# Kernel tuning notes

Measured on AMD Instinct MI355X. Metric: run time of the kernel, lower is better.

The kernel has to match this reference:

```python
import jax, jax.numpy as jnp
import numpy as np

EMBED_DIM = 128
NUM_SYMBOLS = 200000
PAD_IDX = NUM_SYMBOLS
K_NEIGHBORS = 10
PROCESS_STEPS = 4
D_MODEL = 2 * EMBED_DIM   # 256
D_INNER = 2 * D_MODEL     # 512
LSTM_HID = 2 * D_MODEL    # 512
B, F_SUP, MAX_K = 4096, 5, 64


def setup_inputs() -> dict:
    key = jax.random.key(0)
    ks = jax.random.split(key, 40)
    f = lambda i, shape, s=0.05: jax.random.normal(ks[i], shape, jnp.float32) * s
    inp = {}
    inp['query'] = jax.random.randint(ks[0], (B, 2), 0, NUM_SYMBOLS)
    inp['support'] = jax.random.randint(ks[1], (F_SUP, 2), 0, NUM_SYMBOLS)
    inp['q_l1'] = jax.random.randint(ks[2], (B, MAX_K, 2), 0, NUM_SYMBOLS + 1)
    inp['q_deg_l'] = jax.random.randint(ks[3], (B,), 0, 100)
    inp['q_r1'] = jax.random.randint(ks[4], (B, MAX_K, 2), 0, NUM_SYMBOLS + 1)
    inp['q_deg_r'] = jax.random.randint(ks[5], (B,), 0, 100)
    inp['s_l1'] = jax.random.randint(ks[6], (F_SUP, MAX_K, 2), 0, NUM_SYMBOLS + 1)
    inp['s_deg_l'] = jax.random.randint(ks[7], (F_SUP,), 0, 100)
    inp['s_r1'] = jax.random.randint(ks[8], (F_SUP, MAX_K, 2), 0, NUM_SYMBOLS + 1)
    inp['s_deg_r'] = jax.random.randint(ks[9], (F_SUP,), 0, 100)
    # learned parameters
    inp['symbol_emb'] = f(10, (NUM_SYMBOLS + 1, EMBED_DIM), 0.1).at[PAD_IDX].set(0.0)
    inp['gcn_w_w'] = f(11, (EMBED_DIM, 2 * EMBED_DIM))
    inp['gcn_w_b'] = jnp.zeros((EMBED_DIM,), jnp.float32)
    inp['gcn_b'] = jnp.zeros((EMBED_DIM,), jnp.float32)
    inp['g1_w'] = f(12, (EMBED_DIM // 2, EMBED_DIM))
    inp['g1_b'] = jnp.zeros((EMBED_DIM // 2,), jnp.float32)
    inp['ln1_g'] = jnp.ones((EMBED_DIM // 2,), jnp.float32)
    inp['ln1_b'] = jnp.zeros((EMBED_DIM // 2,), jnp.float32)
    inp['g2_w'] = f(13, (1, EMBED_DIM // 2))
    inp['g2_b'] = jnp.zeros((1,), jnp.float32)
    inp['gate_temp'] = jnp.array(1.0, jnp.float32)
    inp['se_p1_w'] = f(14, (D_INNER, D_MODEL))
    inp['se_p1_b'] = jnp.zeros((D_INNER,), jnp.float32)
    inp['se_p2_w'] = f(15, (D_MODEL, D_INNER))
    inp['se_p2_b'] = jnp.zeros((D_MODEL,), jnp.float32)
    inp['se_ln_g'] = jnp.ones((D_MODEL,), jnp.float32)
    inp['se_ln_b'] = jnp.zeros((D_MODEL,), jnp.float32)
    inp['w_ih'] = f(16, (4 * LSTM_HID, D_MODEL))
    inp['w_hh'] = f(17, (4 * LSTM_HID, LSTM_HID))
    inp['b_ih'] = jnp.zeros((4 * LSTM_HID,), jnp.float32)
    inp['b_hh'] = jnp.zeros((4 * LSTM_HID,), jnp.float32)
    return inp


def _layernorm(x, g, b, eps=1e-5):
    m = jnp.mean(x, axis=-1, keepdims=True)
    v = jnp.var(x, axis=-1, keepdims=True)
    return (x - m) / jnp.sqrt(v + eps) * g + b


def _l2norm(x):
    return x / jnp.maximum(jnp.linalg.norm(x, axis=-1, keepdims=True), 1e-12)


def _neighbor_encoder(conn, deg, self_ids, p):
    emb = p['symbol_emb']
    rel, ent = conn[:, :, 0], conn[:, :, 1]
    rel_emb = emb[rel]            # [n, K, D] gather
    ent_emb = emb[ent]            # [n, K, D]
    self_emb = emb[self_ids]      # [n, D]
    sim = jnp.einsum('nd,nkd->nk', _l2norm(self_emb), _l2norm(ent_emb))
    is_pad = (rel == PAD_IDX).astype(jnp.float32)
    sim = sim - is_pad * 1e9
    k = min(K_NEIGHBORS, conn.shape[1])
    _, k_idx = jax.lax.top_k(sim, k)
    bidx = jnp.arange(conn.shape[0])[:, None]
    k_mask = jnp.zeros(sim.shape, jnp.float32).at[bidx, k_idx].set(1.0)[..., None]
    concat = jnp.concatenate([rel_emb, ent_emb], axis=-1)   # [n, K, 2D]
    proj = jax.nn.leaky_relu(concat @ p['gcn_w_w'].T + p['gcn_w_b'] + p['gcn_b'], 0.01)
    valid = (1.0 - is_pad[..., None]) * k_mask
    denom = jnp.maximum(jnp.sum(valid, axis=1), 1.0)
    agg = jnp.sum((proj * k_mask) * valid, axis=1) / denom   # [n, D]
    h = jax.nn.relu(_layernorm(agg @ p['g1_w'].T + p['g1_b'], p['ln1_g'], p['ln1_b']))
    logit = h @ p['g2_w'].T + p['g2_b']                      # [n, 1]
    temp = jnp.clip(p['gate_temp'], 0.1, 5.0)
    gate = jax.nn.sigmoid(logit / temp) * (deg > 0).astype(jnp.float32)[:, None]
    return jnp.tanh(self_emb + gate * agg)


def _support_encoder(x, p):
    h = jax.nn.relu(x @ p['se_p1_w'].T + p['se_p1_b'])
    h = h @ p['se_p2_w'].T + p['se_p2_b']
    return _layernorm(h + x, p['se_ln_g'], p['se_ln_b'])


def _query_encoder(support, query, p):
    n = query.shape[0]
    h_r0 = jnp.zeros((n, LSTM_HID), jnp.float32)
    c0 = jnp.zeros((n, LSTM_HID), jnp.float32)

    def step(carry, _):
        h_r, c = carry
        gates = query @ p['w_ih'].T + p['b_ih'] + h_r @ p['w_hh'].T + p['b_hh']
        i, f, g, o = jnp.split(gates, 4, axis=-1)
        c = jax.nn.sigmoid(f) * c + jax.nn.sigmoid(i) * jnp.tanh(g)
        h_ = jax.nn.sigmoid(o) * jnp.tanh(c)
        h = query + h_[:, :D_MODEL]
        attn = jax.nn.softmax(h @ support.T, axis=1)
        r = attn @ support
        return (jnp.concatenate([h, r], axis=-1), c), None

    (h_r, _), _ = jax.lax.scan(step, (h_r0, c0), None, length=PROCESS_STEPS)
    return h_r[:, :D_MODEL]


def reference(query, support, q_l1, q_deg_l, q_r1, q_deg_r, s_l1, s_deg_l, s_r1, s_deg_r,
              symbol_emb, gcn_w_w, gcn_w_b, gcn_b, g1_w, g1_b, ln1_g, ln1_b, g2_w, g2_b,
              gate_temp, se_p1_w, se_p1_b, se_p2_w, se_p2_b, se_ln_g, se_ln_b,
              w_ih, w_hh, b_ih, b_hh):
    p = dict(symbol_emb=symbol_emb, gcn_w_w=gcn_w_w, gcn_w_b=gcn_w_b, gcn_b=gcn_b,
             g1_w=g1_w, g1_b=g1_b, ln1_g=ln1_g, ln1_b=ln1_b, g2_w=g2_w, g2_b=g2_b,
             gate_temp=gate_temp, se_p1_w=se_p1_w, se_p1_b=se_p1_b, se_p2_w=se_p2_w,
             se_p2_b=se_p2_b, se_ln_g=se_ln_g, se_ln_b=se_ln_b,
             w_ih=w_ih, w_hh=w_hh, b_ih=b_ih, b_hh=b_hh)
    q_left = _neighbor_encoder(q_l1, q_deg_l, query[:, 0], p)
    q_right = _neighbor_encoder(q_r1, q_deg_r, query[:, 1], p)
    query_vec = jnp.concatenate([q_left, q_right], axis=-1)      # [B, 2D]
    s_left = _neighbor_encoder(s_l1, s_deg_l, support[:, 0], p)
    s_right = _neighbor_encoder(s_r1, s_deg_r, support[:, 1], p)
    support_vec = jnp.concatenate([s_left, s_right], axis=-1)    # [F, 2D]
    support_g = jnp.mean(_support_encoder(support_vec, p), axis=0, keepdims=True)  # [1, 2D]
    query_enc = _support_encoder(query_vec, p)                   # [B, 2D]
    query_g = _query_encoder(support_g, query_enc, p)            # [B, 2D]
    return jnp.sum(query_g * support_g, axis=1)                  # [B]
```

## Files before the change

kernel.cpp:

```cpp
#include <hip/hip_runtime.h>
#include <math.h>

#define BQ 4096
#define F_SUP 5
#define MAXK 64
#define ED 128
#define DM 256
#define DI 512
#define LH 512
#define NG 2048
#define PADX 200000
#define KNB 10
#define MROWS 82048
#define MREAL 82020
#define MQ 4224

typedef unsigned short u16;
typedef __attribute__((ext_vector_type(8))) short short8;
typedef __attribute__((ext_vector_type(4))) float floatx4;

__device__ __forceinline__ float sigf(float x) { return 1.0f / (1.0f + __expf(-x)); }
__device__ __forceinline__ float tanh_fast(float x) {
  float a = fabsf(x);
  float e = __expf(-2.0f * a);
  float t = (1.0f - e) / (1.0f + e);
  return copysignf(t, x);
}
__device__ __forceinline__ u16 f2bf(float f) {
  unsigned u = __float_as_uint(f);
  unsigned r = (u + 0x7FFFu + ((u >> 16) & 1u)) >> 16;
  return (u16)r;
}
__device__ __forceinline__ float bf2f(u16 u) {
  return __uint_as_float(((unsigned)u) << 16);
}
__device__ __forceinline__ void gl2lds16(const void* g, void* l) {
  __builtin_amdgcn_global_load_lds(
      (const __attribute__((address_space(1))) void*)g,
      (__attribute__((address_space(3))) void*)l, 16, 0, 0);
}

__global__ __launch_bounds__(256) void nbr_topk_kernel(
    const int* __restrict__ query, const int* __restrict__ support,
    const int* __restrict__ q_l1, const int* __restrict__ q_r1,
    const int* __restrict__ s_l1, const int* __restrict__ s_r1,
    const float* __restrict__ emb,
    int* __restrict__ idxA, int* __restrict__ meta)
{
  __shared__ int relS[64], entS[64];
  __shared__ __align__(16) float sE[128];
  __shared__ float simS[64];
  __shared__ int selS[16];
  __shared__ int cntS;
  __shared__ float nsS;

  int tid = threadIdx.x;
  int b = blockIdx.x;
  const int* conn; int self_id;
  if (b < BQ)              { int i = b;              conn = q_l1 + i*(MAXK*2); self_id = query[2*i];   }
  else if (b < 2*BQ)       { int i = b - BQ;         conn = q_r1 + i*(MAXK*2); self_id = query[2*i+1]; }
  else if (b < 2*BQ+F_SUP) { int i = b - 2*BQ;       conn = s_l1 + i*(MAXK*2); self_id = support[2*i]; }
  else                     { int i = b - 2*BQ-F_SUP; conn = s_r1 + i*(MAXK*2); self_id = support[2*i+1]; }

  if (tid < 128) {
    int v = conn[tid];
    if (tid & 1) entS[tid >> 1] = v; else relS[tid >> 1] = v;
    sE[tid] = emb[(long)self_id * ED + tid];
  }
  __syncthreads();
  if (tid < 64) {
    float v = sE[tid]*sE[tid] + sE[tid+64]*sE[tid+64];
    #pragma unroll
    for (int off = 1; off < 64; off <<= 1) v += __shfl_xor(v, off);
    if (tid == 0) nsS = fmaxf(sqrtf(v), 1e-12f);
  }
  __syncthreads();

  {
    int k = tid >> 2, part = tid & 3;
    const float* er = emb + (long)entS[k] * ED + part * 32;
    const float* sr = &sE[part * 32];
    float dot = 0.f, sq = 0.f;
    #pragma unroll
    for (int j = 0; j < 32; j += 4) {
      float4 e = *(const float4*)(er + j);
      float4 s = *(const float4*)(sr + j);
      dot += e.x*s.x + e.y*s.y + e.z*s.z + e.w*s.w;
      sq  += e.x*e.x + e.y*e.y + e.z*e.z + e.w*e.w;
    }
    dot += __shfl_xor(dot, 1); dot += __shfl_xor(dot, 2);
    sq  += __shfl_xor(sq, 1);  sq  += __shfl_xor(sq, 2);
    if (part == 0) {
      float ne = fmaxf(sqrtf(sq), 1e-12f);
      float sim = dot / (nsS * ne);
      if (relS[k] == PADX) sim -= 1e9f;
      simS[k] = sim;
    }
  }
  __syncthreads();

  if (tid < 64) {
    float mys = simS[tid];
    int rank = 0;
    #pragma unroll
    for (int j = 0; j < 64; ++j) {
      float s = simS[j];
      rank += ((s > mys) || (s == mys && j < tid)) ? 1 : 0;
    }
    bool val = (rank < KNB) && (relS[tid] != PADX);
    unsigned long long vm = __ballot(val ? 1 : 0);
    if (val) {
      int pos = __popcll(vm & ((1ull << tid) - 1ull));
      selS[pos] = tid;
    }
    if (tid == 0) { cntS = __popcll(vm); meta[b] = __popcll(vm); }
  }
  __syncthreads();

  int cnt = cntS;
  long base = (long)b * 10;
  if (tid < 2 * KNB) {
    int kk = tid >> 1, h = tid & 1;
    int id = PADX;
    if (kk < cnt) { int k = selS[kk]; id = h ? entS[k] : relS[k]; }
    idxA[(base + kk) * 2 + h] = id;
  }
  if (b == 0 && tid >= 128 && tid < 128 + 2 * (MROWS - MREAL)) {
    idxA[(long)MREAL * 2 + (tid - 128)] = PADX;
  }
}

__global__ __launch_bounds__(256) void proj_gather_gemm(
    const int* __restrict__ idxA, const float* __restrict__ emb,
    const u16* __restrict__ W, u16* __restrict__ proj)
{
  __shared__ u16 As[128 * 32];
  __shared__ u16 Bs[128 * 32];
  __shared__ int idxS[256];
  int tid = threadIdx.x;
  int bm = blockIdx.x;
  idxS[tid] = idxA[bm * 256 + tid];
  int lane = tid & 63, wave = tid >> 6;
  int wm = (wave & 1) * 64, wn = (wave >> 1) * 64;
  int col = lane & 15, quad = lane >> 4;
  int r = tid >> 1, part = tid & 1;

  floatx4 acc[4][4];
  #pragma unroll
  for (int i = 0; i < 4; ++i)
    #pragma unroll
    for (int j = 0; j < 4; ++j) { floatx4 z = {0.f,0.f,0.f,0.f}; acc[i][j] = z; }
  __syncthreads();

  for (int k0 = 0; k0 < 256; k0 += 32) {
    int half = k0 >> 7, koff = k0 & 127;
    #pragma unroll
    for (int t = 0; t < 2; ++t) {
      int c = t * 256 + tid;
      int rb = c >> 2, o = c & 3;
      int og = o ^ (rb & 3);
      gl2lds16(W + (long)rb * 256 + k0 + og * 8, &Bs[(size_t)c * 8]);
    }
    {
      int id = idxS[r * 2 + half];
      const float* src = emb + (long)id * ED + koff + part * 16;
      float4 f0 = *(const float4*)(src);
      float4 f1 = *(const float4*)(src + 4);
      float4 f2 = *(const float4*)(src + 8);
      float4 f3 = *(const float4*)(src + 12);
      short8 s0, s1;
      s0[0]=(short)f2bf(f0.x); s0[1]=(short)f2bf(f0.y); s0[2]=(short)f2bf(f0.z); s0[3]=(short)f2bf(f0.w);
      s0[4]=(short)f2bf(f1.x); s0[5]=(short)f2bf(f1.y); s0[6]=(short)f2bf(f1.z); s0[7]=(short)f2bf(f1.w);
      s1[0]=(short)f2bf(f2.x); s1[1]=(short)f2bf(f2.y); s1[2]=(short)f2bf(f2.z); s1[3]=(short)f2bf(f2.w);
      s1[4]=(short)f2bf(f3.x); s1[5]=(short)f2bf(f3.y); s1[6]=(short)f2bf(f3.z); s1[7]=(short)f2bf(f3.w);
      int o0 = 2 * part, o1 = 2 * part + 1;
      *(short8*)&As[(size_t)(r * 4 + (o0 ^ (r & 3))) * 8] = s0;
      *(short8*)&As[(size_t)(r * 4 + (o1 ^ (r & 3))) * 8] = s1;
    }
    __syncthreads();
    short8 af[4], bfr[4];
    #pragma unroll
    for (int i = 0; i < 4; ++i) {
      int ra = wm + i * 16 + col;
      af[i] = *(const short8*)&As[(size_t)(ra * 4 + (quad ^ (ra & 3))) * 8];
      int rb = wn + i * 16 + col;
      bfr[i] = *(const short8*)&Bs[(size_t)(rb * 4 + (quad ^ (rb & 3))) * 8];
    }
    #pragma unroll
    for (int i = 0; i < 4; ++i)
      #pragma unroll
      for (int j = 0; j < 4; ++j)
        acc[i][j] = __builtin_amdgcn_mfma_f32_16x16x32_bf16(af[i], bfr[j], acc[i][j], 0, 0, 0);
    __syncthreads();
  }
  int gm0 = bm * 128 + wm + quad * 4;
  int gn0 = wn + col;
  #pragma unroll
  for (int i = 0; i < 4; ++i)
    #pragma unroll
    for (int j = 0; j < 4; ++j)
      #pragma unroll
      for (int rr = 0; rr < 4; ++rr)
        proj[(long)(gm0 + i * 16 + rr) * 128 + gn0 + j * 16] = f2bf(acc[i][j][rr]);
}

__global__ __launch_bounds__(128) void nbr_post_kernel(
    const int* __restrict__ query, const int* __restrict__ support,
    const int* __restrict__ q_deg_l, const int* __restrict__ q_deg_r,
    const int* __restrict__ s_deg_l, const int* __restrict__ s_deg_r,
    const float* __restrict__ emb,
    const u16* __restrict__ proj, const int* __restrict__ meta,
    const float* __restrict__ gcn_w_b, const float* __restrict__ gcn_b,
    const float* __restrict__ g1_w, const float* __restrict__ g1_b,
    const float* __restrict__ ln1_g, const float* __restrict__ ln1_b,
    const float* __restrict__ g2_w, const float* __restrict__ g2_b,
    const float* __restrict__ gate_temp,
    float* __restrict__ qv, u16* __restrict__ qv_bf)
{
  __shared__ __align__(16) float aggS[128];
  __shared__ float sEs[128];
  __shared__ float gateS;
  int tid = threadIdx.x, b = blockIdx.x;
  int deg, self_id, row, colb;
  if (b < BQ)              { int i = b;              deg = q_deg_l[i]; self_id = query[2*i];     row = i;        colb = 0;  }
  else if (b < 2*BQ)       { int i = b - BQ;         deg = q_deg_r[i]; self_id = query[2*i+1];   row = i;        colb = ED; }
  else if (b < 2*BQ+F_SUP) { int i = b - 2*BQ;       deg = s_deg_l[i]; self_id = support[2*i];   row = BQ + i;   colb = 0;  }
  else                     { int i = b - 2*BQ-F_SUP; deg = s_deg_r[i]; self_id = support[2*i+1]; row = BQ + i;   colb = ED; }
  float* outp = qv + (long)row * DM + colb;
  u16*  outpb = qv_bf + (long)row * DM + colb;

  int cnt = meta[b];
  float denom = fmaxf((float)cnt, 1.0f);
  float bsum = gcn_w_b[tid] + gcn_b[tid];
  float agg = 0.f;
  long pbase = (long)b * 10;
  for (int kk = 0; kk < cnt; ++kk) {
    float z = bf2f(proj[(pbase + kk) * 128 + tid]) + bsum;
    z = (z >= 0.f) ? z : 0.01f * z;
    agg += z;
  }
  agg /= denom;
  aggS[tid] = agg;
  sEs[tid] = emb[(long)self_id * ED + tid];
  __syncthreads();

  if (tid < 64) {
    int e = tid;
    const float4* g1r = (const float4*)(g1_w + e * ED);
    float y = g1_b[e];
    #pragma unroll 8
    for (int j = 0; j < 32; ++j) {
      float4 w = g1r[j];
      float4 a = *(const float4*)&aggS[j * 4];
      y += w.x*a.x + w.y*a.y + w.z*a.z + w.w*a.w;
    }
    float s = y;
    #pragma unroll
    for (int off = 1; off < 64; off <<= 1) s += __shfl_xor(s, off);
    float mean = s * (1.0f / 64.0f);
    float dv = y - mean;
    float s2 = dv * dv;
    #pragma unroll
    for (int off = 1; off < 64; off <<= 1) s2 += __shfl_xor(s2, off);
    float var = s2 * (1.0f / 64.0f);
    float hv = dv / sqrtf(var + 1e-5f) * ln1_g[e] + ln1_b[e];
    hv = fmaxf(hv, 0.f);
    float lp = hv * g2_w[e];
    #pragma unroll
    for (int off = 1; off < 64; off <<= 1) lp += __shfl_xor(lp, off);
    if (e == 0) {
      float logit = lp + g2_b[0];
      float temp = fminf(fmaxf(gate_temp[0], 0.1f), 5.0f);
      float gate = 1.0f / (1.0f + expf(-logit / temp));
      if (deg <= 0) gate = 0.f;
      gateS = gate;
    }
  }
  __syncthreads();
  float o = tanhf(sEs[tid] + gateS * aggS[tid]);
  outp[tid] = o;
  outpb[tid] = f2bf(o);
}

__global__ __launch_bounds__(256) void mfma_gemm(
    const u16* __restrict__ A, int lda,
    const u16* __restrict__ W, int ldw,
    int N, int K,
    float* __restrict__ Cout, u16* __restrict__ Cbf,
    const float* __restrict__ bias0,
    const u16* __restrict__ gqin,
    u16* __restrict__ gqout,
    int relu, int lstm_mode,
    float* __restrict__ cstate, const float* __restrict__ qe,
    u16* __restrict__ hbf)
{
  __shared__ u16 As[128 * 32];
  __shared__ u16 Bs[128 * 32];
  int tid = threadIdx.x;
  int nb = N >> 7;
  int bn = blockIdx.x % nb, bm = blockIdx.x / nb;
  int lane = tid & 63, wave = tid >> 6;
  int wm = (wave & 1) * 64, wn = (wave >> 1) * 64;
  int col = lane & 15, quad = lane >> 4;

  u16 gqa[64]; float cpv[16]; float qev[16]; float scv[4];
  int u = 0; long fb = 0;
  if (lstm_mode) {
    u = bn * 32 + (wave >> 1) * 16 + col;
    fb = ((long)blockIdx.x * 4 + wave) * 64 + lane;
    #pragma unroll
    for (int j = 0; j < 4; ++j)
      scv[j] = bias0[bn * 128 + (wave >> 1) * 64 + j * 16 + col];
    if (lstm_mode == 1) {
      const short8* gp = (const short8*)(gqin + fb * 64);
      #pragma unroll
      for (int t = 0; t < 8; ++t) *(short8*)&gqa[t * 8] = gp[t];
      const float4* cp = (const float4*)(cstate + fb * 16);
      #pragma unroll
      for (int t = 0; t < 4; ++t) *(float4*)&cpv[t * 4] = cp[t];
    }
    if (u < DM) {
      #pragma unroll
      for (int i = 0; i < 4; ++i)
        #pragma unroll
        for (int r = 0; r < 4; ++r) {
          int m = bm * 128 + (wave & 1) * 64 + i * 16 + quad * 4 + r;
          qev[i * 4 + r] = qe[(long)m * DM + u];
        }
    }
  }

  floatx4 acc[4][4];
  #pragma unroll
  for (int i = 0; i < 4; ++i)
    #pragma unroll
    for (int j = 0; j < 4; ++j) { floatx4 z = {0.f,0.f,0.f,0.f}; acc[i][j] = z; }

  for (int k0 = 0; k0 < K; k0 += 32) {
    #pragma unroll
    for (int t = 0; t < 2; ++t) {
      int c = t * 256 + tid;
      int r = c >> 2, o = c & 3;
      int og = o ^ (r & 3);
      gl2lds16(A + (long)(bm * 128 + r) * lda + k0 + og * 8, &As[(size_t)c * 8]);
      gl2lds16(W + (long)(bn * 128 + r) * ldw + k0 + og * 8, &Bs[(size_t)c * 8]);
    }
    __syncthreads();
    short8 af[4], bfr[4];
    #pragma unroll
    for (int i = 0; i < 4; ++i) {
      int ra = wm + i * 16 + col;
      af[i] = *(const short8*)&As[(size_t)(ra * 4 + (quad ^ (ra & 3))) * 8];
      int rb = wn + i * 16 + col;
      bfr[i] = *(const short8*)&Bs[(size_t)(rb * 4 + (quad ^ (rb & 3))) * 8];
    }
    #pragma unroll
    for (int i = 0; i < 4; ++i)
      #pragma unroll
      for (int j = 0; j < 4; ++j)
        acc[i][j] = __builtin_amdgcn_mfma_f32_16x16x32_bf16(af[i], bfr[j], acc[i][j], 0, 0, 0);
    __syncthreads();
  }

  if (lstm_mode) {
    float cnew[16];
    #pragma unroll
    for (int i = 0; i < 4; ++i) {
      #pragma unroll
      for (int r = 0; r < 4; ++r) {
        float gI = acc[i][0][r] + scv[0];
        float gF = acc[i][1][r] + scv[1];
        float gG = acc[i][2][r] + scv[2];
        float gO = acc[i][3][r] + scv[3];
        if (lstm_mode == 1) {
          gI += bf2f(gqa[(i * 4 + 0) * 4 + r]);
          gF += bf2f(gqa[(i * 4 + 1) * 4 + r]);
          gG += bf2f(gqa[(i * 4 + 2) * 4 + r]);
          gO += bf2f(gqa[(i * 4 + 3) * 4 + r]);
        }
        float cp = (lstm_mode == 2) ? 0.f : cpv[i * 4 + r];
        float cn = sigf(gF) * cp + sigf(gI) * tanh_fast(gG);
        cnew[i * 4 + r] = cn;
        if (u < DM) {
          int m = bm * 128 + (wave & 1) * 64 + i * 16 + quad * 4 + r;
          hbf[(long)m * DM + u] = f2bf(qev[i * 4 + r] + sigf(gO) * tanh_fast(cn));
        }
      }
    }
    {
      float4* cp = (float4*)(cstate + fb * 16);
      #pragma unroll
      for (int t = 0; t < 4; ++t) cp[t] = *(float4*)&cnew[t * 4];
    }
    if (lstm_mode == 2) {
      u16 ga[64];
      #pragma unroll
      for (int i = 0; i < 4; ++i)
        #pragma unroll
        for (int j = 0; j < 4; ++j)
          #pragma unroll
          for (int r = 0; r < 4; ++r)
            ga[(i * 4 + j) * 4 + r] = f2bf(acc[i][j][r] + scv[j]);
      short8* gp = (short8*)(gqout + fb * 64);
      #pragma unroll
      for (int t = 0; t < 8; ++t) gp[t] = *(short8*)&ga[t * 8];
    }
  } else {
    int gm0 = bm * 128 + wm + quad * 4;
    int gn0 = bn * 128 + wn + col;
    #pragma unroll
    for (int i = 0; i < 4; ++i) {
      #pragma unroll
      for (int j = 0; j < 4; ++j) {
        int n = gn0 + j * 16;
        #pragma unroll
        for (int r = 0; r < 4; ++r) {
          int m = gm0 + i * 16 + r;
          float v = acc[i][j][r];
          if (bias0) v += bias0[n];
          if (relu) v = fmaxf(v, 0.f);
          if (Cout) Cout[(long)m * N + n] = v;
          if (Cbf)  Cbf[(long)m * N + n] = f2bf(v);
        }
      }
    }
  }
}

__global__ void prep_cast(
    const float* __restrict__ p1, const float* __restrict__ p2,
    const float* __restrict__ gcnw, const float* __restrict__ wih,
    const float* __restrict__ whh, const float* __restrict__ bih,
    const float* __restrict__ bhh,
    u16* __restrict__ p1b, u16* __restrict__ p2b, u16* __restrict__ gcnb,
    u16* __restrict__ wihb, u16* __restrict__ whhb, float* __restrict__ bihh)
{
  int gid = blockIdx.x * 256 + threadIdx.x;
  if (gid < 131072) { p1b[gid] = f2bf(p1[gid]); }
  else if (gid < 262144) { int i = gid - 131072; p2b[i] = f2bf(p2[i]); }
  else if (gid < 294912) { int i = gid - 262144; gcnb[i] = f2bf(gcnw[i]); }
  else if (gid < 819200) {
    int i = gid - 294912; int p = i >> 8, k = i & 255;
    int g = (p >> 4) & 3, uu = (p >> 7) * 32 + ((p >> 6) & 1) * 16 + (p & 15);
    int n = g * 512 + uu;
    wihb[i] = f2bf(wih[(long)n * DM + k]);
  } else if (gid < 1343488) {
    int i = gid - 819200; int p = i >> 8, k = i & 255;
    int g = (p >> 4) & 3, uu = (p >> 7) * 32 + ((p >> 6) & 1) * 16 + (p & 15);
    int n = g * 512 + uu;
    whhb[i] = f2bf(whh[(long)n * LH + k]);
  } else if (gid < 1345536) {
    int p = gid - 1343488;
    int g = (p >> 4) & 3, uu = (p >> 7) * 32 + ((p >> 6) & 1) * 16 + (p & 15);
    int n = g * 512 + uu;
    bihh[p] = bih[n] + bhh[n];
  }
}

__global__ __launch_bounds__(256) void ln_residual_kernel(
    const float* __restrict__ h2buf, const float* __restrict__ xbuf,
    const float* __restrict__ lng, const float* __restrict__ lnb,
    float* __restrict__ out, u16* __restrict__ outb)
{
  __shared__ float red[4];
  int r = blockIdx.x, tid = threadIdx.x;
  float v = h2buf[(long)r * DM + tid] + xbuf[(long)r * DM + tid];
  float s = v;
  #pragma unroll
  for (int off = 1; off < 64; off <<= 1) s += __shfl_xor(s, off);
  if ((tid & 63) == 0) red[tid >> 6] = s;
  __syncthreads();
  float mean = (red[0] + red[1] + red[2] + red[3]) * (1.0f / 256.0f);
  __syncthreads();
  float dv = v - mean;
  float s2 = dv * dv;
  #pragma unroll
  for (int off = 1; off < 64; off <<= 1) s2 += __shfl_xor(s2, off);
  if ((tid & 63) == 0) red[tid >> 6] = s2;
  __syncthreads();
  float var = (red[0] + red[1] + red[2] + red[3]) * (1.0f / 256.0f);
  float o = dv / sqrtf(var + 1e-5f) * lng[tid] + lnb[tid];
  out[(long)r * DM + tid] = o;
  outb[(long)r * DM + tid] = f2bf(o);
}

__global__ __launch_bounds__(256) void scorr_kernel(
    const float* __restrict__ qe, const float* __restrict__ whh,
    float* __restrict__ sg, float* __restrict__ s_corr_perm)
{
  __shared__ float sgS[DM];
  int tid = threadIdx.x;
  {
    float v = 0.f;
    #pragma unroll
    for (int r = 0; r < F_SUP; ++r) v += qe[(long)(BQ + r) * DM + tid];
    v *= (1.0f / (float)F_SUP);
    sgS[tid] = v;
    if (blockIdx.x == 0) sg[tid] = v;
  }
  __syncthreads();
  int wave = tid >> 6, lane = tid & 63;
  int n = blockIdx.x * 4 + wave;
  float4 w = *(const float4*)(whh + (long)n * LH + DM + lane * 4);
  float4 s = *(const float4*)&sgS[lane * 4];
  float d = w.x*s.x + w.y*s.y + w.z*s.z + w.w*s.w;
  #pragma unroll
  for (int off = 1; off < 64; off <<= 1) d += __shfl_xor(d, off);
  if (lane == 0) {
    int g = n >> 9, uu = n & 511;
    int p = (uu >> 5) * 128 + ((uu >> 4) & 1) * 64 + g * 16 + (uu & 15);
    s_corr_perm[p] = d;
  }
}

__global__ __launch_bounds__(256) void final_dot_kernel(
    const u16* __restrict__ h, const float* __restrict__ sg, float* __restrict__ out)
{
  __shared__ float red[4];
  int m = blockIdx.x, tid = threadIdx.x;
  float v = bf2f(h[(long)m * DM + tid]) * sg[tid];
  #pragma unroll
  for (int off = 1; off < 64; off <<= 1) v += __shfl_xor(v, off);
  if ((tid & 63) == 0) red[tid >> 6] = v;
  __syncthreads();
  if (tid == 0) out[m] = red[0] + red[1] + red[2] + red[3];
}

extern "C" void kernel_launch(void* const* d_in, const int* in_sizes, int n_in,
                              void* d_out, int out_size, void* d_ws, size_t ws_size,
                              hipStream_t stream)
{
  const int*   query    = (const int*)  d_in[0];
  const int*   support  = (const int*)  d_in[1];
  const int*   q_l1     = (const int*)  d_in[2];
  const int*   q_deg_l  = (const int*)  d_in[3];
  const int*   q_r1     = (const int*)  d_in[4];
  const int*   q_deg_r  = (const int*)  d_in[5];
  const int*   s_l1     = (const int*)  d_in[6];
  const int*   s_deg_l  = (const int*)  d_in[7];
  const int*   s_r1     = (const int*)  d_in[8];
  const int*   s_deg_r  = (const int*)  d_in[9];
  const float* symbol_emb = (const float*)d_in[10];
  const float* gcn_w_w  = (const float*)d_in[11];
  const float* gcn_w_b  = (const float*)d_in[12];
  const float* gcn_b    = (const float*)d_in[13];
  const float* g1_w     = (const float*)d_in[14];
  const float* g1_b     = (const float*)d_in[15];
  const float* ln1_g    = (const float*)d_in[16];
  const float* ln1_b    = (const float*)d_in[17];
  const float* g2_w     = (const float*)d_in[18];
  const float* g2_b     = (const float*)d_in[19];
  const float* gate_temp= (const float*)d_in[20];
  const float* se_p1_w  = (const float*)d_in[21];
  const float* se_p1_b  = (const float*)d_in[22];
  const float* se_p2_w  = (const float*)d_in[23];
  const float* se_p2_b  = (const float*)d_in[24];
  const float* se_ln_g  = (const float*)d_in[25];
  const float* se_ln_b  = (const float*)d_in[26];
  const float* w_ih     = (const float*)d_in[27];
  const float* w_hh     = (const float*)d_in[28];
  const float* b_ih     = (const float*)d_in[29];
  const float* b_hh     = (const float*)d_in[30];

  float* ws = (float*)d_ws;
  size_t off = 0;
  float* projF   = ws + off; off += (size_t)MROWS * 128 / 2;
  float* idxF    = ws + off; off += (size_t)MROWS * 2;
  float* qv      = ws + off; off += (size_t)MQ * DM;
  float* qe      = ws + off; off += (size_t)MQ * DM;
  float* qv_bfF  = ws + off; off += (size_t)MQ * DM / 2;
  float* qe_bfF  = ws + off; off += (size_t)MQ * DM / 2;
  float* h1bF    = ws + off; off += (size_t)MQ * DI / 2;
  float* H2      = ws + off; off += (size_t)MQ * DM;
  float* gqbF    = ws + off; off += (size_t)BQ * NG / 2;
  float* cstate  = ws + off; off += (size_t)BQ * LH;
  float* hbf0F   = ws + off; off += (size_t)BQ * DM / 2;
  float* hbf1F   = ws + off; off += (size_t)BQ * DM / 2;
  float* p1bF    = ws + off; off += 131072 / 2;
  float* p2bF    = ws + off; off += 131072 / 2;
  float* gcnbF   = ws + off; off += 32768 / 2;
  float* wihbF   = ws + off; off += 524288 / 2;
  float* whhbF   = ws + off; off += 524288 / 2;
  float* bihh    = ws + off; off += 2048;
  float* sg      = ws + off; off += 256;
  float* s_corr  = ws + off; off += 2048;
  float* metaF   = ws + off; off += 8448;

  u16* proj   = (u16*)projF;
  int* idxA   = (int*)idxF;
  u16* qv_bf  = (u16*)qv_bfF;
  u16* qe_bf  = (u16*)qe_bfF;
  u16* H1_bf  = (u16*)h1bF;
  u16* gq_fr  = (u16*)gqbF;
  u16* hbf0   = (u16*)hbf0F;
  u16* hbf1   = (u16*)hbf1F;
  u16* p1b    = (u16*)p1bF;
  u16* p2b    = (u16*)p2bF;
  u16* gcnb   = (u16*)gcnbF;
  u16* wihb   = (u16*)wihbF;
  u16* whhb   = (u16*)whhbF;
  int* meta   = (int*)metaF;

  prep_cast<<<5256, 256, 0, stream>>>(se_p1_w, se_p2_w, gcn_w_w, w_ih, w_hh, b_ih, b_hh,
                                      p1b, p2b, gcnb, wihb, whhb, bihh);

  nbr_topk_kernel<<<2 * BQ + 2 * F_SUP, 256, 0, stream>>>(
      query, support, q_l1, q_r1, s_l1, s_r1, symbol_emb, idxA, meta);

  proj_gather_gemm<<<MROWS / 128, 256, 0, stream>>>(idxA, symbol_emb, gcnb, proj);

  nbr_post_kernel<<<2 * BQ + 2 * F_SUP, 128, 0, stream>>>(
      query, support, q_deg_l, q_deg_r, s_deg_l, s_deg_r, symbol_emb,
      proj, meta, gcn_w_b, gcn_b, g1_w, g1_b, ln1_g, ln1_b, g2_w, g2_b, gate_temp,
      qv, qv_bf);

  mfma_gemm<<<(MQ / 128) * (DI / 128), 256, 0, stream>>>(qv_bf, 256, p1b, 256, DI, 256,
      nullptr, H1_bf, se_p1_b, nullptr, nullptr, 1, 0, nullptr, nullptr, nullptr);
  mfma_gemm<<<(MQ / 128) * (DM / 128), 256, 0, stream>>>(H1_bf, 512, p2b, 512, DM, 512,
      H2, nullptr, se_p2_b, nullptr, nullptr, 0, 0, nullptr, nullptr, nullptr);
  ln_residual_kernel<<<BQ + F_SUP, 256, 0, stream>>>(H2, qv, se_ln_g, se_ln_b, qe, qe_bf);

  scorr_kernel<<<512, 256, 0, stream>>>(qe, w_hh, sg, s_corr);

  mfma_gemm<<<(BQ / 128) * (NG / 128), 256, 0, stream>>>(qe_bf, 256, wihb, 256, NG, 256,
      nullptr, nullptr, bihh, nullptr, gq_fr, 0, 2, cstate, qe, hbf0);

  mfma_gemm<<<(BQ / 128) * (NG / 128), 256, 0, stream>>>(hbf0, 256, whhb, 256, NG, 256,
      nullptr, nullptr, s_corr, gq_fr, nullptr, 0, 1, cstate, qe, hbf1);
  mfma_gemm<<<(BQ / 128) * (NG / 128), 256, 0, stream>>>(hbf1, 256, whhb, 256, NG, 256,
      nullptr, nullptr, s_corr, gq_fr, nullptr, 0, 1, cstate, qe, hbf0);
  mfma_gemm<<<(BQ / 128) * (NG / 128), 256, 0, stream>>>(hbf0, 256, whhb, 256, NG, 256,
      nullptr, nullptr, s_corr, gq_fr, nullptr, 0, 1, cstate, qe, hbf1);

  final_dot_kernel<<<BQ, 256, 0, stream>>>(hbf1, sg, (float*)d_out);
}
```

Before: 427.6 us.

## Split neighbor top-k into a barrier-free similarity kernel and a wave-level rank kernel

The fused top-k kernel is split in two. The first kernel computes cosine similarities with a single barrier, interleaved coalesced float4 loads, and no division by the self-embedding norm, since a positive scale does not change the ranking. It writes the similarities to a global buffer. The second kernel ranks them with one wave per row using shuffles and writes the selected index pairs. This removes several block barriers and most idle threads, at the cost of an extra launch and a global round trip for the similarity buffer.

```diff
diff --git a/kernel.cpp b/kernel.cpp
--- a/kernel.cpp
+++ b/kernel.cpp
@@ -40,93 +40,84 @@
       (__attribute__((address_space(3))) void*)l, 16, 0, 0);
 }
 
-__global__ __launch_bounds__(256) void nbr_topk_kernel(
+__global__ __launch_bounds__(256) void nbr_sim_kernel(
     const int* __restrict__ query, const int* __restrict__ support,
     const int* __restrict__ q_l1, const int* __restrict__ q_r1,
     const int* __restrict__ s_l1, const int* __restrict__ s_r1,
-    const float* __restrict__ emb,
-    int* __restrict__ idxA, int* __restrict__ meta)
-{
-  __shared__ int relS[64], entS[64];
+    const float* __restrict__ emb, float* __restrict__ simG)
+{
   __shared__ __align__(16) float sE[128];
-  __shared__ float simS[64];
-  __shared__ int selS[16];
-  __shared__ int cntS;
-  __shared__ float nsS;
-
   int tid = threadIdx.x;
   int b = blockIdx.x;
   const int* conn; int self_id;
-  if (b < BQ)              { int i = b;              conn = q_l1 + i*(MAXK*2); self_id = query[2*i];   }
-  else if (b < 2*BQ)       { int i = b - BQ;         conn = q_r1 + i*(MAXK*2); self_id = query[2*i+1]; }
-  else if (b < 2*BQ+F_SUP) { int i = b - 2*BQ;       conn = s_l1 + i*(MAXK*2); self_id = support[2*i]; }
-  else                     { int i = b - 2*BQ-F_SUP; conn = s_r1 + i*(MAXK*2); self_id = support[2*i+1]; }
-
-  if (tid < 128) {
-    int v = conn[tid];
-    if (tid & 1) entS[tid >> 1] = v; else relS[tid >> 1] = v;
-    sE[tid] = emb[(long)self_id * ED + tid];
-  }
-  __syncthreads();
-  if (tid < 64) {
-    float v = sE[tid]*sE[tid] + sE[tid+64]*sE[tid+64];
-    #pragma unroll
-    for (int off = 1; off < 64; off <<= 1) v += __shfl_xor(v, off);
-    if (tid == 0) nsS = fmaxf(sqrtf(v), 1e-12f);
-  }
-  __syncthreads();
-
-  {
-    int k = tid >> 2, part = tid & 3;
-    const float* er = emb + (long)entS[k] * ED + part * 32;
-    const float* sr = &sE[part * 32];
-    float dot = 0.f, sq = 0.f;
-    #pragma unroll
-    for (int j = 0; j < 32; j += 4) {
-      float4 e = *(const float4*)(er + j);
-      float4 s = *(const float4*)(sr + j);
-      dot += e.x*s.x + e.y*s.y + e.z*s.z + e.w*s.w;
-      sq  += e.x*e.x + e.y*e.y + e.z*e.z + e.w*e.w;
-    }
-    dot += __shfl_xor(dot, 1); dot += __shfl_xor(dot, 2);
-    sq  += __shfl_xor(sq, 1);  sq  += __shfl_xor(sq, 2);
-    if (part == 0) {
-      float ne = fmaxf(sqrtf(sq), 1e-12f);
-      float sim = dot / (nsS * ne);
-      if (relS[k] == PADX) sim -= 1e9f;
-      simS[k] = sim;
-    }
-  }
-  __syncthreads();
-
-  if (tid < 64) {
-    float mys = simS[tid];
+  if (b < BQ)              { int i = b;              conn = q_l1 + (long)i*(MAXK*2); self_id = query[2*i];   }
+  else if (b < 2*BQ)       { int i = b - BQ;         conn = q_r1 + (long)i*(MAXK*2); self_id = query[2*i+1]; }
+  else if (b < 2*BQ+F_SUP) { int i = b - 2*BQ;       conn = s_l1 + (long)i*(MAXK*2); self_id = support[2*i]; }
+  else                     { int i = b - 2*BQ-F_SUP; conn = s_r1 + (long)i*(MAXK*2); self_id = support[2*i+1]; }
+
+  int k = tid >> 2, part = tid & 3;
+  int2 rc = *(const int2*)(conn + 2 * k);
+  if (tid < 32) *(float4*)&sE[tid * 4] = *(const float4*)(emb + (long)self_id * ED + tid * 4);
+  __syncthreads();
+
+  const float* er = emb + (long)rc.y * ED + part * 4;
+  float dot = 0.f, sq = 0.f;
+  #pragma unroll
+  for (int i = 0; i < 8; ++i) {
+    float4 e = *(const float4*)(er + i * 16);
+    float4 s = *(const float4*)(&sE[i * 16 + part * 4]);
+    dot += e.x*s.x + e.y*s.y + e.z*s.z + e.w*s.w;
+    sq  += e.x*e.x + e.y*e.y + e.z*e.z + e.w*e.w;
+  }
+  dot += __shfl_xor(dot, 1); dot += __shfl_xor(dot, 2);
+  sq  += __shfl_xor(sq, 1);  sq  += __shfl_xor(sq, 2);
+  if (part == 0) {
+    float ne = fmaxf(sqrtf(sq), 1e-12f);
+    float sim = dot / ne;
+    if (rc.x == PADX) sim -= 1e9f;
+    simG[(long)b * 64 + k] = sim;
+  }
+}
+
+__global__ __launch_bounds__(256) void nbr_rank_kernel(
+    const int* __restrict__ q_l1, const int* __restrict__ q_r1,
+    const int* __restrict__ s_l1, const int* __restrict__ s_r1,
+    const float* __restrict__ simG, int* __restrict__ idxA, int* __restrict__ meta)
+{
+  int tid = threadIdx.x;
+  int wave = tid >> 6, lane = tid & 63;
+  int b = blockIdx.x * 4 + wave;
+  if (b < 2 * BQ + 2 * F_SUP) {
+    const int* conn;
+    if (b < BQ)              conn = q_l1 + (long)b * (MAXK*2);
+    else if (b < 2*BQ)       conn = q_r1 + (long)(b - BQ) * (MAXK*2);
+    else if (b < 2*BQ+F_SUP) conn = s_l1 + (long)(b - 2*BQ) * (MAXK*2);
+    else                     conn = s_r1 + (long)(b - 2*BQ - F_SUP) * (MAXK*2);
+
+    float my = simG[(long)b * 64 + lane];
     int rank = 0;
     #pragma unroll
     for (int j = 0; j < 64; ++j) {
-      float s = simS[j];
-      rank += ((s > mys) || (s == mys && j < tid)) ? 1 : 0;
-    }
-    bool val = (rank < KNB) && (relS[tid] != PADX);
+      float s = __shfl(my, j);
+      rank += ((s > my) || (s == my && j < lane)) ? 1 : 0;
+    }
+    int2 rc = *(const int2*)(conn + 2 * lane);
+    bool val = (rank < KNB) && (rc.x != PADX);
     unsigned long long vm = __ballot(val ? 1 : 0);
+    int cnt = __popcll(vm);
+    long base = (long)b * 10;
     if (val) {
-      int pos = __popcll(vm & ((1ull << tid) - 1ull));
-      selS[pos] = tid;
-    }
-    if (tid == 0) { cntS = __popcll(vm); meta[b] = __popcll(vm); }
-  }
-  __syncthreads();
-
-  int cnt = cntS;
-  long base = (long)b * 10;
-  if (tid < 2 * KNB) {
-    int kk = tid >> 1, h = tid & 1;
-    int id = PADX;
-    if (kk < cnt) { int k = selS[kk]; id = h ? entS[k] : relS[k]; }
-    idxA[(base + kk) * 2 + h] = id;
-  }
-  if (b == 0 && tid >= 128 && tid < 128 + 2 * (MROWS - MREAL)) {
-    idxA[(long)MREAL * 2 + (tid - 128)] = PADX;
+      int pos = __popcll(vm & ((1ull << lane) - 1ull));
+      *(int2*)(idxA + (base + pos) * 2) = rc;
+    }
+    if (lane >= cnt && lane < KNB) {
+      int2 pp; pp.x = PADX; pp.y = PADX;
+      *(int2*)(idxA + (base + lane) * 2) = pp;
+    }
+    if (lane == 0) meta[b] = cnt;
+  }
+  if (blockIdx.x == 0 && tid < 2 * (MROWS - MREAL)) {
+    idxA[(long)MREAL * 2 + tid] = PADX;
   }
 }
 
@@ -585,6 +576,7 @@
   float* sg      = ws + off; off += 256;
   float* s_corr  = ws + off; off += 2048;
   float* metaF   = ws + off; off += 8448;
+  float* simF    = ws + off; off += (size_t)8448 * 64;
 
   u16* proj   = (u16*)projF;
   int* idxA   = (int*)idxF;
@@ -604,8 +596,11 @@
   prep_cast<<<5256, 256, 0, stream>>>(se_p1_w, se_p2_w, gcn_w_w, w_ih, w_hh, b_ih, b_hh,
                                       p1b, p2b, gcnb, wihb, whhb, bihh);
 
-  nbr_topk_kernel<<<2 * BQ + 2 * F_SUP, 256, 0, stream>>>(
-      query, support, q_l1, q_r1, s_l1, s_r1, symbol_emb, idxA, meta);
+  nbr_sim_kernel<<<2 * BQ + 2 * F_SUP, 256, 0, stream>>>(
+      query, support, q_l1, q_r1, s_l1, s_r1, symbol_emb, simF);
+
+  nbr_rank_kernel<<<(2 * BQ + 2 * F_SUP + 3) / 4, 256, 0, stream>>>(
+      q_l1, q_r1, s_l1, s_r1, simF, idxA, meta);
 
   proj_gather_gemm<<<MROWS / 128, 256, 0, stream>>>(idxA, symbol_emb, gcnb, proj);
 
```

Measured after the change: 428.1 us. No clear change (+0.1%).
